# Optimization experiments

Hardware: AMD Instinct MI355X
Metric: run time of the kernel (lower is better)

Reference implementation:

```python
import jax, jax.numpy as jnp
import numpy as np

DIM = 256
HEAD_DIM = 32
GRID = 8
EPS_GN = 1e-6
EPS_LN = 1e-5


def groupnorm1(x, w, b):
    # GroupNorm(1, C): normalize over (C,H,W) per sample, per-channel affine.
    m = jnp.mean(x, axis=(1, 2, 3), keepdims=True)
    v = jnp.var(x, axis=(1, 2, 3), keepdims=True)
    xn = (x - m) * jax.lax.rsqrt(v + EPS_GN)
    return xn * w[None, :, None, None] + b[None, :, None, None]


def conv1x1(x, w, b=None):
    # 1x1 conv as channel matmul; w: [out, in]
    y = jnp.einsum('bchw,oc->bohw', x, w)
    if b is not None:
        y = y + b[None, :, None, None]
    return y


def setup_inputs() -> dict:
    key = jax.random.key(0)
    ks = jax.random.split(key, 8)
    C = DIM
    s = 0.02
    return {
        'x': jax.random.normal(ks[0], (4, C, 64, 64), dtype=jnp.float32),
        'norm_w': jnp.ones((C,), jnp.float32),
        'norm_b': jnp.zeros((C,), jnp.float32),
        'qkv_w': jax.random.normal(ks[1], (3 * C, C), jnp.float32) * s,
        'qkv_b': jnp.zeros((3 * C,), jnp.float32),
        'proj_w': jax.random.normal(ks[2], (C, C), jnp.float32) * s,
        'proj_b': jnp.zeros((C,), jnp.float32),
        'grid_norm_w': jnp.ones((C,), jnp.float32),
        'grid_norm_b': jnp.zeros((C,), jnp.float32),
        'pm_ln_w': jnp.ones((4 * C,), jnp.float32),
        'pm_ln_b': jnp.zeros((4 * C,), jnp.float32),
        'pm_red_w': jax.random.normal(ks[3], (C, 4 * C), jnp.float32) * s,
        'ds_norm_w': jnp.ones((C,), jnp.float32),
        'ds_norm_b': jnp.zeros((C,), jnp.float32),
        'q_w': jax.random.normal(ks[4], (C, C), jnp.float32) * s,
        'q_b': jnp.zeros((C,), jnp.float32),
        'kv_w': jax.random.normal(ks[5], (2 * C, C), jnp.float32) * s,
        'kv_b': jnp.zeros((2 * C,), jnp.float32),
    }


def reference(x, norm_w, norm_b, qkv_w, qkv_b, proj_w, proj_b,
              grid_norm_w, grid_norm_b, pm_ln_w, pm_ln_b, pm_red_w,
              ds_norm_w, ds_norm_b, q_w, q_b, kv_w, kv_b):
    B, C, H, W = x.shape
    hd = HEAD_DIM
    nh = C // hd
    gs = GRID
    gh, gw = H // gs, W // gs
    scale = hd ** -0.5

    # ---- local windowed (grid) attention ----
    qkv = conv1x1(groupnorm1(x, norm_w, norm_b), qkv_w, qkv_b)  # [B,3C,H,W]
    qkv = qkv.reshape(B, 3, nh, hd, gh, gs, gw, gs)
    qkv = qkv.transpose(1, 0, 2, 4, 6, 5, 7, 3).reshape(3, -1, gs * gs, hd)
    q, k, v = qkv[0], qkv[1], qkv[2]
    attn = jax.nn.softmax(jnp.einsum('nqd,nkd->nqk', q * scale, k), axis=-1)
    gx = jnp.einsum('nqk,nkd->nqd', attn, v)
    gx = gx.reshape(B, nh, gh, gw, gs, gs, hd)
    gx = gx.transpose(0, 1, 6, 2, 4, 3, 5).reshape(B, C, H, W)
    grid_x = groupnorm1(x + gx, grid_norm_w, grid_norm_b)

    t = grid_x.transpose(0, 2, 3, 1)  # BHWC
    m = jnp.concatenate([t[:, 0::2, 0::2], t[:, 1::2, 0::2],
                         t[:, 0::2, 1::2], t[:, 1::2, 1::2]], axis=-1)
    m = m.reshape(B, (H // 2) * (W // 2), 4 * C)
    mu = jnp.mean(m, axis=-1, keepdims=True)
    var = jnp.var(m, axis=-1, keepdims=True)
    m = (m - mu) * jax.lax.rsqrt(var + EPS_LN) * pm_ln_w + pm_ln_b
    m = m @ pm_red_w.T  # [B, HW/4, C]
    pm = m.reshape(B, H // 2, W // 2, C).transpose(0, 3, 1, 2)

    # ---- global attention (full q attends to pooled kv) ----
    ds = groupnorm1(pm, ds_norm_w, ds_norm_b)
    qg = conv1x1(grid_x, q_w, q_b).reshape(B, nh, hd, H * W).transpose(0, 1, 3, 2)
    kvg = conv1x1(ds, kv_w, kv_b).reshape(B, 2, nh, hd, (H // 2) * (W // 2))
    kvg = kvg.transpose(1, 0, 2, 4, 3)
    kg, vg = kvg[0], kvg[1]
    attn2 = jax.nn.softmax(jnp.einsum('bnqd,bnkd->bnqk', qg * scale, kg), axis=-1)
    go = jnp.einsum('bnqk,bnkd->bnqd', attn2, vg)
    go = go.transpose(0, 1, 3, 2).reshape(B, C, H, W)
    global_x = go + grid_x

    # drop=0.0 -> identity
    return conv1x1(global_x, proj_w, proj_b)
```

## Files before the change

kernel.cpp:

```cpp
#include <hip/hip_runtime.h>
#include <hip/hip_bf16.h>

#define BATCH 4
#define CDIM 256
#define HWSZ 4096
#define P2 1024
#define SCALE 0.17677669529663687f
#define LOG2E 1.4426950408889634f
#define SCL2 (SCALE * LOG2E)
#define EPS_GN 1e-6f
#define EPS_LN 1e-5f
#define MFIX 8.0f
#define MFIX2 (MFIX * LOG2E)

typedef short v8s __attribute__((ext_vector_type(8)));
typedef float v4f __attribute__((ext_vector_type(4)));

__device__ __forceinline__ unsigned short f2bf(float f) {
    __hip_bfloat16 h = __float2bfloat16(f);
    return *reinterpret_cast<unsigned short*>(&h);
}
__device__ __forceinline__ float bf2f(unsigned short u) {
    return __uint_as_float(((unsigned int)u) << 16);
}
__device__ __forceinline__ float bflo(unsigned int u) {
    return __uint_as_float(u << 16);
}
__device__ __forceinline__ float bfhi(unsigned int u) {
    return __uint_as_float(u & 0xffff0000u);
}
__device__ __forceinline__ unsigned int pack2(float lo, float hi) {
    return (unsigned int)f2bf(lo) | ((unsigned int)f2bf(hi) << 16);
}
__device__ __forceinline__ unsigned int tpack2(float lo, float hi) {
    return (__float_as_uint(lo) >> 16) | (__float_as_uint(hi) & 0xffff0000u);
}
__device__ __forceinline__ float fexp2(float x) {
#if __has_builtin(__builtin_amdgcn_exp2f)
    return __builtin_amdgcn_exp2f(x);
#else
    return exp2f(x);
#endif
}
__device__ __forceinline__ uint2 expack2(v4f s, float& sum) {
    float a = fexp2(s[0] - MFIX2);
    float b = fexp2(s[1] - MFIX2);
    float c = fexp2(s[2] - MFIX2);
    float d = fexp2(s[3] - MFIX2);
    sum += (a + b) + (c + d);
    return make_uint2(tpack2(a, b), tpack2(c, d));
}
__device__ __forceinline__ v8s u4v8(uint2 a, uint2 b) {
    union { unsigned int u[4]; v8s v; } r;
    r.u[0] = a.x; r.u[1] = a.y; r.u[2] = b.x; r.u[3] = b.y;
    return r.v;
}
__device__ __forceinline__ int vperm(int j) {
    return (j & 0x23) | ((j & 0x0C) << 1) | ((j & 0x10) >> 2);
}
__device__ __forceinline__ void async16(void* lds, const void* g) {
    __builtin_amdgcn_global_load_lds(
        (const __attribute__((address_space(1))) unsigned int*)g,
        (__attribute__((address_space(3))) unsigned int*)lds, 16, 0, 0);
}

__global__ void gn_partial4(const float* __restrict__ a, const unsigned short* __restrict__ a2bf,
                            int pb4, int nblk, float* __restrict__ part)
{
    int bb  = blockIdx.x / nblk;
    int blk = blockIdx.x % nblk;
    const float* pa = a + (size_t)bb * pb4 * 4;
    const unsigned short* pa2 = a2bf ? a2bf + (size_t)bb * pb4 * 4 : nullptr;
    int tid = threadIdx.x;
    float s = 0.f, s2 = 0.f;
    for (int i = blk * 256 + tid; i < pb4; i += nblk * 256) {
        float4 v = *(const float4*)(pa + (size_t)i * 4);
        if (pa2) {
            uint2 g = *(const uint2*)(pa2 + (size_t)i * 4);
            v.x += bflo(g.x); v.y += bfhi(g.x);
            v.z += bflo(g.y); v.w += bfhi(g.y);
        }
        s += (v.x + v.y) + (v.z + v.w);
        s2 += fmaf(v.x, v.x, fmaf(v.y, v.y, fmaf(v.z, v.z, v.w * v.w)));
    }
    __shared__ float ls[256], ls2[256];
    ls[tid] = s; ls2[tid] = s2; __syncthreads();
    for (int off = 128; off > 0; off >>= 1) {
        if (tid < off) { ls[tid] += ls[tid + off]; ls2[tid] += ls2[tid + off]; }
        __syncthreads();
    }
    if (tid == 0) {
        part[blockIdx.x * 2]     = ls[0];
        part[blockIdx.x * 2 + 1] = ls2[0];
    }
}

__global__ void cast_weights(const float* __restrict__ w0, const float* __restrict__ w1,
                             const float* __restrict__ w2, const float* __restrict__ w3,
                             const float* __restrict__ w4, unsigned short* __restrict__ dst)
{
    int i = blockIdx.x * 256 + threadIdx.x;
    int idx = i * 4;
    const float* src; int off;
    if      (idx < 196608) { src = w0; off = 0; }
    else if (idx < 458752) { src = w1; off = 196608; }
    else if (idx < 589824) { src = w2; off = 458752; }
    else if (idx < 655360) { src = w3; off = 589824; }
    else                   { src = w4; off = 655360; }
    float4 v = *(const float4*)(src + idx - off);
    *(uint2*)(dst + idx) = make_uint2(pack2(v.x, v.y), pack2(v.z, v.w));
}

__global__ __launch_bounds__(256) void tnc(
    const float* __restrict__ A, const unsigned short* __restrict__ A2b,
    const float* __restrict__ part, int nblk, float inv_n, float eps,
    const float* __restrict__ nw, const float* __restrict__ nb,
    unsigned short* __restrict__ dst, int P)
{
    int b = blockIdx.z, c0 = blockIdx.y * 64, p0 = blockIdx.x * 64;
    __shared__ float ld[64][65];
    __shared__ float sstat[2];
    int t = threadIdx.x;
    if (t < 64) {
        float s = 0.f, s2 = 0.f;
        if (t < nblk) {
            s  = part[(b * nblk + t) * 2];
            s2 = part[(b * nblk + t) * 2 + 1];
        }
        #pragma unroll
        for (int off = 32; off > 0; off >>= 1) {
            s  += __shfl_down(s, off);
            s2 += __shfl_down(s2, off);
        }
        if (t == 0) {
            float mval = s * inv_n;
            float var  = s2 * inv_n - mval * mval;
            sstat[0] = mval;
            sstat[1] = rsqrtf(var + eps);
        }
    }
    __syncthreads();
    float mean = sstat[0], rstd = sstat[1];
    {
        int ch = t >> 2, pq = (t & 3) * 16;
        size_t base = ((size_t)b * 256 + c0 + ch) * P + p0 + pq;
        float4 f0 = *(const float4*)(A + base);
        float4 f1 = *(const float4*)(A + base + 4);
        float4 f2 = *(const float4*)(A + base + 8);
        float4 f3 = *(const float4*)(A + base + 12);
        if (A2b) {
            const unsigned short* ap = A2b + base;
            uint4 q0 = *(const uint4*)(ap);
            uint4 q1 = *(const uint4*)(ap + 8);
            f0.x += bflo(q0.x); f0.y += bfhi(q0.x); f0.z += bflo(q0.y); f0.w += bfhi(q0.y);
            f1.x += bflo(q0.z); f1.y += bfhi(q0.z); f1.z += bflo(q0.w); f1.w += bfhi(q0.w);
            f2.x += bflo(q1.x); f2.y += bfhi(q1.x); f2.z += bflo(q1.y); f2.w += bfhi(q1.y);
            f3.x += bflo(q1.z); f3.y += bfhi(q1.z); f3.z += bflo(q1.w); f3.w += bfhi(q1.w);
        }
        float wv = nw[c0 + ch];
        float sw = rstd * wv;
        float sb = nb[c0 + ch] - mean * rstd * wv;
        ld[ch][pq + 0]  = f0.x * sw + sb; ld[ch][pq + 1]  = f0.y * sw + sb;
        ld[ch][pq + 2]  = f0.z * sw + sb; ld[ch][pq + 3]  = f0.w * sw + sb;
        ld[ch][pq + 4]  = f1.x * sw + sb; ld[ch][pq + 5]  = f1.y * sw + sb;
        ld[ch][pq + 6]  = f1.z * sw + sb; ld[ch][pq + 7]  = f1.w * sw + sb;
        ld[ch][pq + 8]  = f2.x * sw + sb; ld[ch][pq + 9]  = f2.y * sw + sb;
        ld[ch][pq + 10] = f2.z * sw + sb; ld[ch][pq + 11] = f2.w * sw + sb;
        ld[ch][pq + 12] = f3.x * sw + sb; ld[ch][pq + 13] = f3.y * sw + sb;
        ld[ch][pq + 14] = f3.z * sw + sb; ld[ch][pq + 15] = f3.w * sw + sb;
    }
    __syncthreads();
    {
        int p = t >> 2, cb = (t & 3) * 16;
        unsigned int u[8];
        #pragma unroll
        for (int j = 0; j < 8; j++)
            u[j] = pack2(ld[cb + 2 * j][p], ld[cb + 2 * j + 1][p]);
        unsigned short* dp = dst + ((size_t)b * P + p0 + p) * 256 + c0 + cb;
        *(uint4*)(dp)     = make_uint4(u[0], u[1], u[2], u[3]);
        *(uint4*)(dp + 8) = make_uint4(u[4], u[5], u[6], u[7]);
    }
}

template<int MODE>
__global__ __launch_bounds__(256, 3) void gemm_bf16(
    const unsigned short* __restrict__ actT,
    const unsigned short* __restrict__ Wb,
    const float* __restrict__ bias,
    float* __restrict__ out,
    unsigned short* __restrict__ aux1,
    unsigned short* __restrict__ aux2,
    int K, int P, int OC, float oscale)
{
    int b  = blockIdx.z;
    int p0 = blockIdx.x * 128;
    int m0 = blockIdx.y * 128;
    int tid = threadIdx.x;
    int w = tid >> 6, lane = tid & 63;
    int lm = lane & 15, lg = lane >> 4;
    int wm = w >> 1, wp = w & 1;
    int l8 = lane >> 3, cc = lane & 7;

    __shared__ __align__(16) unsigned short Wt[128 * 64];
    __shared__ __align__(16) unsigned short At[128 * 64];

    const unsigned short* actB = actT + (size_t)b * P * K;

    v4f acc[4][4];
    #pragma unroll
    for (int i = 0; i < 4; i++)
        #pragma unroll
        for (int j = 0; j < 4; j++) acc[i][j] = (v4f){0.f, 0.f, 0.f, 0.f};

    for (int ks = 0; ks < K; ks += 64) {
        #pragma unroll
        for (int i = 0; i < 4; i++) {
            int ml = w * 32 + i * 8 + l8;
            int g = cc ^ (ml & 7);
            async16(&Wt[ml * 64], Wb + (size_t)(m0 + ml) * K + ks + g * 8);
        }
        #pragma unroll
        for (int i = 0; i < 4; i++) {
            int pl = w * 32 + i * 8 + l8;
            int g = cc ^ (pl & 7);
            async16(&At[pl * 64], actB + (size_t)(p0 + pl) * K + ks + g * 8);
        }
        __syncthreads();
        #pragma unroll
        for (int kk = 0; kk < 2; kk++) {
            v8s af[4], bfv[4];
            #pragma unroll
            for (int mt = 0; mt < 4; mt++) {
                int m = wm * 64 + mt * 16 + lm;
                int ch = (kk * 4 + lg) ^ (m & 7);
                af[mt] = *(const v8s*)&Wt[m * 64 + ch * 8];
            }
            #pragma unroll
            for (int pt = 0; pt < 4; pt++) {
                int p = wp * 64 + pt * 16 + lm;
                int ch = (kk * 4 + lg) ^ (p & 7);
                bfv[pt] = *(const v8s*)&At[p * 64 + ch * 8];
            }
            #pragma unroll
            for (int mt = 0; mt < 4; mt++)
                #pragma unroll
                for (int pt = 0; pt < 4; pt++)
                    acc[mt][pt] = __builtin_amdgcn_mfma_f32_16x16x32_bf16(
                        af[mt], bfv[pt], acc[mt][pt], 0, 0, 0);
        }
        __syncthreads();
    }

    if constexpr (MODE == 1) {
        if (m0 < 512) {
            #pragma unroll
            for (int mt = 0; mt < 4; mt++) {
                int mch = m0 + wm * 64 + mt * 16 + lg * 4;
                float4 bs = *(const float4*)(bias + mch);
                #pragma unroll
                for (int pt = 0; pt < 4; pt++) {
                    int p = p0 + wp * 64 + pt * 16 + lm;
                    unsigned int u0 = pack2(acc[mt][pt][0] + bs.x, acc[mt][pt][1] + bs.y);
                    unsigned int u1 = pack2(acc[mt][pt][2] + bs.z, acc[mt][pt][3] + bs.w);
                    *(uint2*)(aux1 + ((size_t)(b * 4096 + p) * 512 + mch)) = make_uint2(u0, u1);
                }
            }
        } else {
            #pragma unroll
            for (int mt = 0; mt < 4; mt++) {
                #pragma unroll
                for (int r = 0; r < 4; r++) {
                    int mch = m0 + wm * 64 + mt * 16 + lg * 4 + r;
                    float bsv = bias[mch];
                    unsigned short* orow = aux2 + ((size_t)b * 256 + (mch - 512)) * 4096
                                           + p0 + wp * 64;
                    #pragma unroll
                    for (int pt = 0; pt < 4; pt++)
                        orow[pt * 16 + lm] = f2bf(acc[mt][pt][r] + bsv);
                }
            }
        }
    } else if constexpr (MODE == 2) {
        #pragma unroll
        for (int mt = 0; mt < 4; mt++) {
            int ch = m0 + wm * 64 + mt * 16 + lg * 4;
            int head = ch >> 5, d = ch & 31;
            float4 bs = *(const float4*)(bias + ch);
            #pragma unroll
            for (int pt = 0; pt < 4; pt++) {
                int p = p0 + wp * 64 + pt * 16 + lm;
                unsigned int u0 = pack2((acc[mt][pt][0] + bs.x) * oscale,
                                        (acc[mt][pt][1] + bs.y) * oscale);
                unsigned int u1 = pack2((acc[mt][pt][2] + bs.z) * oscale,
                                        (acc[mt][pt][3] + bs.w) * oscale);
                *(uint2*)(aux1 + ((size_t)(b * 8 + head) * P + p) * 32 + d) = make_uint2(u0, u1);
            }
        }
    } else if constexpr (MODE == 3) {
        #pragma unroll
        for (int mt = 0; mt < 4; mt++) {
            int ch = m0 + wm * 64 + mt * 16 + lg * 4;
            if (ch < 256) {
                int head = ch >> 5, d = ch & 31;
                float4 bs = *(const float4*)(bias + ch);
                #pragma unroll
                for (int pt = 0; pt < 4; pt++) {
                    int p = p0 + wp * 64 + pt * 16 + lm;
                    unsigned int u0 = pack2(acc[mt][pt][0] + bs.x, acc[mt][pt][1] + bs.y);
                    unsigned int u1 = pack2(acc[mt][pt][2] + bs.z, acc[mt][pt][3] + bs.w);
                    *(uint2*)(aux1 + ((size_t)(b * 8 + head) * P + p) * 32 + d) = make_uint2(u0, u1);
                }
            } else {
                int v = ch - 256;
                int head = v >> 5, d0 = v & 31;
                #pragma unroll
                for (int pt = 0; pt < 4; pt++) {
                    int p = p0 + wp * 64 + pt * 16 + lm;
                    int pos = (p & ~63) | vperm(p & 63);
                    #pragma unroll
                    for (int r = 0; r < 4; r++)
                        aux2[((size_t)(b * 8 + head) * 32 + d0 + r) * P + pos] =
                            f2bf(acc[mt][pt][r] + bias[ch + r]);
                }
            }
        }
    } else {
        #pragma unroll
        for (int mt = 0; mt < 4; mt++) {
            #pragma unroll
            for (int r = 0; r < 4; r++) {
                int m = m0 + wm * 64 + mt * 16 + lg * 4 + r;
                float bs = bias ? bias[m] : 0.f;
                float* orow = out + (size_t)b * OC * P + (size_t)m * P + p0 + wp * 64;
                #pragma unroll
                for (int pt = 0; pt < 4; pt++)
                    orow[pt * 16 + lm] = acc[mt][pt][r] + bs;
            }
        }
    }
}

__global__ __launch_bounds__(256, 4) void local_attn_mfma(
    const unsigned short* __restrict__ qkp,
    const unsigned short* __restrict__ vbb,
    unsigned short* __restrict__ gxb)
{
    int win = blockIdx.x;
    int gxc = win & 7, gy = (win >> 3) & 7, h = (win >> 6) & 7, b = win >> 9;
    int w = threadIdx.x >> 6, lane = threadIdx.x & 63;
    int m = lane & 15, g = lane >> 4;

    int rowbase = (gy * 8) * 64 + gxc * 8;
    const unsigned short* qkb = qkp + (size_t)b * 4096 * 512;
    const unsigned short* vbase = vbb + (size_t)b * 256 * 4096;

    int tq = w * 16 + m;
    int pq = rowbase + (tq >> 3) * 64 + (tq & 7);
    v8s qf = *(const v8s*)(qkb + (size_t)pq * 512 + h * 32 + g * 8);

    v8s ka[4];
    #pragma unroll
    for (int kt = 0; kt < 4; kt++) {
        int tk = kt * 16 + m;
        int pk = rowbase + (tk >> 3) * 64 + (tk & 7);
        ka[kt] = *(const v8s*)(qkb + (size_t)pk * 512 + 256 + h * 32 + g * 8);
    }
    v8s vb[2][2];
    #pragma unroll
    for (int c = 0; c < 2; c++)
        #pragma unroll
        for (int dt = 0; dt < 2; dt++) {
            const unsigned short* vp = vbase + (size_t)(h * 32 + dt * 16 + m) * 4096
                              + rowbase + (4 * c + (g >> 1)) * 64 + (g & 1) * 4;
            vb[c][dt] = u4v8(*(const uint2*)vp, *(const uint2*)(vp + 128));
        }

    const v4f zf = {0.f, 0.f, 0.f, 0.f};
    v4f s[4];
    #pragma unroll
    for (int kt = 0; kt < 4; kt++)
        s[kt] = __builtin_amdgcn_mfma_f32_16x16x32_bf16(ka[kt], qf, zf, 0, 0, 0);

    float lsum = 0.f;
    uint2 u0, u1, u2, u3;
    {
        v4f sc;
        #pragma unroll
        for (int r = 0; r < 4; r++) sc[r] = s[0][r] * SCL2;
        u0 = expack2(sc, lsum);
        #pragma unroll
        for (int r = 0; r < 4; r++) sc[r] = s[1][r] * SCL2;
        u1 = expack2(sc, lsum);
        #pragma unroll
        for (int r = 0; r < 4; r++) sc[r] = s[2][r] * SCL2;
        u2 = expack2(sc, lsum);
        #pragma unroll
        for (int r = 0; r < 4; r++) sc[r] = s[3][r] * SCL2;
        u3 = expack2(sc, lsum);
    }
    lsum += __shfl_xor(lsum, 16);
    lsum += __shfl_xor(lsum, 32);
    float inv = 1.f / lsum;

    v8s pa0 = u4v8(u0, u1), pa1 = u4v8(u2, u3);
    v4f o0 = zf, o1 = zf;
    o0 = __builtin_amdgcn_mfma_f32_16x16x32_bf16(pa0, vb[0][0], o0, 0, 0, 0);
    o1 = __builtin_amdgcn_mfma_f32_16x16x32_bf16(pa0, vb[0][1], o1, 0, 0, 0);
    o0 = __builtin_amdgcn_mfma_f32_16x16x32_bf16(pa1, vb[1][0], o0, 0, 0, 0);
    o1 = __builtin_amdgcn_mfma_f32_16x16x32_bf16(pa1, vb[1][1], o1, 0, 0, 0);

    float invq[4];
    #pragma unroll
    for (int r = 0; r < 4; r++) invq[r] = __shfl(inv, g * 4 + r);

    int t0 = w * 16 + g * 4;
    int px0 = rowbase + (t0 >> 3) * 64 + (t0 & 7);
    unsigned short* op0 = gxb + ((size_t)b * 256 + h * 32 + m) * 4096 + px0;
    *(uint2*)op0 = make_uint2(pack2(o0[0] * invq[0], o0[1] * invq[1]),
                              pack2(o0[2] * invq[2], o0[3] * invq[3]));
    unsigned short* op1 = gxb + ((size_t)b * 256 + h * 32 + 16 + m) * 4096 + px0;
    *(uint2*)op1 = make_uint2(pack2(o1[0] * invq[0], o1[1] * invq[1]),
                              pack2(o1[2] * invq[2], o1[3] * invq[3]));
}

__global__ __launch_bounds__(256) void patch_merge_ln2(
    const unsigned short* __restrict__ gxT,
    const float* __restrict__ lnw, const float* __restrict__ lnb,
    unsigned short* __restrict__ mn)
{
    int pix = blockIdx.x;
    int b = pix >> 10, op = pix & 1023;
    int oh = op >> 5, ow = op & 31;
    int t = threadIdx.x;
    const unsigned short* base = gxT + (size_t)b * 4096 * 256;
    float v[4];
    #pragma unroll
    for (int i = 0; i < 4; i++) {
        int h = 2 * oh + (i & 1);
        int w = 2 * ow + (i >> 1);
        v[i] = bf2f(base[(size_t)(h * 64 + w) * 256 + t]);
    }
    float s  = v[0] + v[1] + v[2] + v[3];
    float s2 = v[0]*v[0] + v[1]*v[1] + v[2]*v[2] + v[3]*v[3];
    __shared__ float ls[256], ls2[256];
    ls[t] = s; ls2[t] = s2; __syncthreads();
    for (int off = 128; off > 0; off >>= 1) {
        if (t < off) { ls[t] += ls[t + off]; ls2[t] += ls2[t + off]; }
        __syncthreads();
    }
    float mu  = ls[0] * (1.f / 1024.f);
    float var = ls2[0] * (1.f / 1024.f) - mu * mu;
    float r = rsqrtf(var + EPS_LN);
    unsigned short* orow = mn + (size_t)pix * 1024;
    #pragma unroll
    for (int i = 0; i < 4; i++) {
        int j = i * 256 + t;
        orow[j] = f2bf((v[i] - mu) * r * lnw[j] + lnb[j]);
    }
}

__global__ __launch_bounds__(256, 2) void global_attn_mfma(
    const unsigned short* __restrict__ qT,
    const unsigned short* __restrict__ kT,
    const unsigned short* __restrict__ vT,
    const unsigned short* __restrict__ gxT,
    unsigned short* __restrict__ projT)
{
    int blk = blockIdx.x;
    int qt = blk & 15, h = (blk >> 4) & 7, b = blk >> 7;
    int bh = b * 8 + h;
    int w = threadIdx.x >> 6, lane = threadIdx.x & 63;
    int m = lane & 15, g = lane >> 4;
    int qbase = qt * 256 + w * 64;

    const unsigned short* qp = qT + ((size_t)bh * 4096 + qbase + m) * 32 + g * 8;
    v8s qf0 = *(const v8s*)(qp);
    v8s qf1 = *(const v8s*)(qp + 16 * 32);
    v8s qf2 = *(const v8s*)(qp + 32 * 32);
    v8s qf3 = *(const v8s*)(qp + 48 * 32);

    const v4f zf = {0.f, 0.f, 0.f, 0.f};
    v4f o00 = zf, o01 = zf, o10 = zf, o11 = zf;
    v4f o20 = zf, o21 = zf, o30 = zf, o31 = zf;
    float l0 = 0.f, l1 = 0.f, l2 = 0.f, l3 = 0.f;

    const unsigned short* kbase = kT + ((size_t)bh * 1024 + m) * 32 + g * 8;
    const unsigned short* vbase = vT + ((size_t)bh * 32 + m) * 1024 + g * 8;

    v8s ka0 = *(const v8s*)(kbase);
    v8s ka1 = *(const v8s*)(kbase + 16 * 32);
    v8s ka2 = *(const v8s*)(kbase + 32 * 32);
    v8s ka3 = *(const v8s*)(kbase + 48 * 32);
    v8s vb0 = *(const v8s*)(vbase);
    v8s vb1 = *(const v8s*)(vbase + 16 * 1024);
    v8s vb2 = *(const v8s*)(vbase + 32);
    v8s vb3 = *(const v8s*)(vbase + 32 + 16 * 1024);

    #pragma unroll 2
    for (int t = 0; t < 16; t++) {
        int kn = (t < 15 ? t + 1 : 15) * 64;
        const unsigned short* kp = kbase + (size_t)kn * 32;
        const unsigned short* vp = vbase + kn;
        v8s nk0 = *(const v8s*)(kp);
        v8s nk1 = *(const v8s*)(kp + 16 * 32);
        v8s nk2 = *(const v8s*)(kp + 32 * 32);
        v8s nk3 = *(const v8s*)(kp + 48 * 32);
        v8s nv0 = *(const v8s*)(vp);
        v8s nv1 = *(const v8s*)(vp + 16 * 1024);
        v8s nv2 = *(const v8s*)(vp + 32);
        v8s nv3 = *(const v8s*)(vp + 32 + 16 * 1024);
        __builtin_amdgcn_sched_barrier(0);

        {
            v4f s0 = __builtin_amdgcn_mfma_f32_16x16x32_bf16(ka0, qf0, zf, 0, 0, 0);
            v4f s1 = __builtin_amdgcn_mfma_f32_16x16x32_bf16(ka1, qf0, zf, 0, 0, 0);
            v4f s2 = __builtin_amdgcn_mfma_f32_16x16x32_bf16(ka2, qf0, zf, 0, 0, 0);
            v4f s3 = __builtin_amdgcn_mfma_f32_16x16x32_bf16(ka3, qf0, zf, 0, 0, 0);
            uint2 a0 = expack2(s0, l0), a1 = expack2(s1, l0);
            uint2 a2 = expack2(s2, l0), a3 = expack2(s3, l0);
            v8s pa0 = u4v8(a0, a1), pa1 = u4v8(a2, a3);
            o00 = __builtin_amdgcn_mfma_f32_16x16x32_bf16(pa0, vb0, o00, 0, 0, 0);
            o01 = __builtin_amdgcn_mfma_f32_16x16x32_bf16(pa0, vb1, o01, 0, 0, 0);
            o00 = __builtin_amdgcn_mfma_f32_16x16x32_bf16(pa1, vb2, o00, 0, 0, 0);
            o01 = __builtin_amdgcn_mfma_f32_16x16x32_bf16(pa1, vb3, o01, 0, 0, 0);
        }
        {
            v4f s0 = __builtin_amdgcn_mfma_f32_16x16x32_bf16(ka0, qf1, zf, 0, 0, 0);
            v4f s1 = __builtin_amdgcn_mfma_f32_16x16x32_bf16(ka1, qf1, zf, 0, 0, 0);
            v4f s2 = __builtin_amdgcn_mfma_f32_16x16x32_bf16(ka2, qf1, zf, 0, 0, 0);
            v4f s3 = __builtin_amdgcn_mfma_f32_16x16x32_bf16(ka3, qf1, zf, 0, 0, 0);
            uint2 a0 = expack2(s0, l1), a1 = expack2(s1, l1);
            uint2 a2 = expack2(s2, l1), a3 = expack2(s3, l1);
            v8s pa0 = u4v8(a0, a1), pa1 = u4v8(a2, a3);
            o10 = __builtin_amdgcn_mfma_f32_16x16x32_bf16(pa0, vb0, o10, 0, 0, 0);
            o11 = __builtin_amdgcn_mfma_f32_16x16x32_bf16(pa0, vb1, o11, 0, 0, 0);
            o10 = __builtin_amdgcn_mfma_f32_16x16x32_bf16(pa1, vb2, o10, 0, 0, 0);
            o11 = __builtin_amdgcn_mfma_f32_16x16x32_bf16(pa1, vb3, o11, 0, 0, 0);
        }
        {
            v4f s0 = __builtin_amdgcn_mfma_f32_16x16x32_bf16(ka0, qf2, zf, 0, 0, 0);
            v4f s1 = __builtin_amdgcn_mfma_f32_16x16x32_bf16(ka1, qf2, zf, 0, 0, 0);
            v4f s2 = __builtin_amdgcn_mfma_f32_16x16x32_bf16(ka2, qf2, zf, 0, 0, 0);
            v4f s3 = __builtin_amdgcn_mfma_f32_16x16x32_bf16(ka3, qf2, zf, 0, 0, 0);
            uint2 a0 = expack2(s0, l2), a1 = expack2(s1, l2);
            uint2 a2 = expack2(s2, l2), a3 = expack2(s3, l2);
            v8s pa0 = u4v8(a0, a1), pa1 = u4v8(a2, a3);
            o20 = __builtin_amdgcn_mfma_f32_16x16x32_bf16(pa0, vb0, o20, 0, 0, 0);
            o21 = __builtin_amdgcn_mfma_f32_16x16x32_bf16(pa0, vb1, o21, 0, 0, 0);
            o20 = __builtin_amdgcn_mfma_f32_16x16x32_bf16(pa1, vb2, o20, 0, 0, 0);
            o21 = __builtin_amdgcn_mfma_f32_16x16x32_bf16(pa1, vb3, o21, 0, 0, 0);
        }
        {
            v4f s0 = __builtin_amdgcn_mfma_f32_16x16x32_bf16(ka0, qf3, zf, 0, 0, 0);
            v4f s1 = __builtin_amdgcn_mfma_f32_16x16x32_bf16(ka1, qf3, zf, 0, 0, 0);
            v4f s2 = __builtin_amdgcn_mfma_f32_16x16x32_bf16(ka2, qf3, zf, 0, 0, 0);
            v4f s3 = __builtin_amdgcn_mfma_f32_16x16x32_bf16(ka3, qf3, zf, 0, 0, 0);
            uint2 a0 = expack2(s0, l3), a1 = expack2(s1, l3);
            uint2 a2 = expack2(s2, l3), a3 = expack2(s3, l3);
            v8s pa0 = u4v8(a0, a1), pa1 = u4v8(a2, a3);
            o30 = __builtin_amdgcn_mfma_f32_16x16x32_bf16(pa0, vb0, o30, 0, 0, 0);
            o31 = __builtin_amdgcn_mfma_f32_16x16x32_bf16(pa0, vb1, o31, 0, 0, 0);
            o30 = __builtin_amdgcn_mfma_f32_16x16x32_bf16(pa1, vb2, o30, 0, 0, 0);
            o31 = __builtin_amdgcn_mfma_f32_16x16x32_bf16(pa1, vb3, o31, 0, 0, 0);
        }

        ka0 = nk0; ka1 = nk1; ka2 = nk2; ka3 = nk3;
        vb0 = nv0; vb1 = nv1; vb2 = nv2; vb3 = nv3;
    }

    float lf[4] = {l0, l1, l2, l3};
    v4f oq0[4] = {o00, o10, o20, o30};
    v4f oq1[4] = {o01, o11, o21, o31};
    #pragma unroll
    for (int qi = 0; qi < 4; qi++) {
        float lfq = lf[qi];
        lfq += __shfl_xor(lfq, 16);
        lfq += __shfl_xor(lfq, 32);
        float inv = 1.f / lfq;
        float invq[4];
        #pragma unroll
        for (int r = 0; r < 4; r++) invq[r] = __shfl(inv, g * 4 + r);
        #pragma unroll
        for (int r = 0; r < 4; r++) {
            size_t row = ((size_t)b * 4096 + qbase + qi * 16 + g * 4 + r) * 256 + h * 32;
            projT[row + m]      = f2bf(bf2f(gxT[row + m])      + oq0[qi][r] * invq[r]);
            projT[row + 16 + m] = f2bf(bf2f(gxT[row + 16 + m]) + oq1[qi][r] * invq[r]);
        }
    }
}

extern "C" void kernel_launch(void* const* d_in, const int* in_sizes, int n_in,
                              void* d_out, int out_size, void* d_ws, size_t ws_size,
                              hipStream_t stream)
{
    const float* x           = (const float*)d_in[0];
    const float* norm_w      = (const float*)d_in[1];
    const float* norm_b      = (const float*)d_in[2];
    const float* qkv_w       = (const float*)d_in[3];
    const float* qkv_b       = (const float*)d_in[4];
    const float* proj_w      = (const float*)d_in[5];
    const float* proj_b      = (const float*)d_in[6];
    const float* grid_norm_w = (const float*)d_in[7];
    const float* grid_norm_b = (const float*)d_in[8];
    const float* pm_ln_w     = (const float*)d_in[9];
    const float* pm_ln_b     = (const float*)d_in[10];
    const float* pm_red_w    = (const float*)d_in[11];
    const float* ds_norm_w   = (const float*)d_in[12];
    const float* ds_norm_b   = (const float*)d_in[13];
    const float* q_w         = (const float*)d_in[14];
    const float* q_b         = (const float*)d_in[15];
    const float* kv_w        = (const float*)d_in[16];
    const float* kv_b        = (const float*)d_in[17];
    float* out = (float*)d_out;

    float* wsf = (float*)d_ws;
    unsigned short* qkp   = (unsigned short*)(wsf);
    unsigned short* vbb   = (unsigned short*)(wsf + 4194304);
    unsigned short* mnb   = (unsigned short*)(wsf);
    unsigned short* kTu   = (unsigned short*)(wsf);
    unsigned short* vTu   = (unsigned short*)(wsf + 524288);
    float* pm             = wsf + 2097152;
    unsigned short* pmT   = (unsigned short*)(wsf + 3145728);
    unsigned short* qTu   = (unsigned short*)(wsf + 10485760);
    unsigned short* gxb   = (unsigned short*)(wsf + 12582912);
    unsigned short* projT = (unsigned short*)(wsf + 12582912);
    unsigned short* xT    = (unsigned short*)(wsf + 16777216);
    unsigned short* gxT   = (unsigned short*)(wsf + 16777216);
    float* part   = wsf + 18874368;
    unsigned short* wbf   = (unsigned short*)(wsf + 18875392);
    unsigned short* wbf_qkv  = wbf;
    unsigned short* wbf_pm   = wbf + 196608;
    unsigned short* wbf_kv   = wbf + 458752;
    unsigned short* wbf_q    = wbf + 589824;
    unsigned short* wbf_proj = wbf + 655360;

    cast_weights<<<704, 256, 0, stream>>>(qkv_w, pm_red_w, kv_w, q_w, proj_w, wbf);
    gn_partial4<<<BATCH * 64, 256, 0, stream>>>(x, nullptr, 262144, 64, part);
    tnc<<<dim3(64, 4, BATCH), 256, 0, stream>>>(
        x, nullptr, part, 64, 1.f / 1048576.f, EPS_GN, norm_w, norm_b, xT, 4096);
    gemm_bf16<1><<<dim3(32, 6, BATCH), 256, 0, stream>>>(
        xT, wbf_qkv, qkv_b, nullptr, qkp, vbb, 256, 4096, 768, 1.f);
    local_attn_mfma<<<2048, 256, 0, stream>>>(qkp, vbb, gxb);
    gn_partial4<<<BATCH * 64, 256, 0, stream>>>(x, gxb, 262144, 64, part);
    tnc<<<dim3(64, 4, BATCH), 256, 0, stream>>>(
        x, gxb, part, 64, 1.f / 1048576.f, EPS_GN, grid_norm_w, grid_norm_b, gxT, 4096);
    patch_merge_ln2<<<4096, 256, 0, stream>>>(gxT, pm_ln_w, pm_ln_b, mnb);
    gemm_bf16<0><<<dim3(8, 2, BATCH), 256, 0, stream>>>(
        mnb, wbf_pm, nullptr, pm, nullptr, nullptr, 1024, 1024, 256, 1.f);
    gn_partial4<<<BATCH * 16, 256, 0, stream>>>(pm, nullptr, 65536, 16, part);
    tnc<<<dim3(16, 4, BATCH), 256, 0, stream>>>(
        pm, nullptr, part, 16, 1.f / 262144.f, EPS_GN, ds_norm_w, ds_norm_b, pmT, 1024);
    gemm_bf16<3><<<dim3(8, 4, BATCH), 256, 0, stream>>>(
        pmT, wbf_kv, kv_b, nullptr, kTu, vTu, 256, 1024, 512, 1.f);
    gemm_bf16<2><<<dim3(32, 2, BATCH), 256, 0, stream>>>(
        gxT, wbf_q, q_b, nullptr, qTu, nullptr, 256, 4096, 256, SCL2);
    global_attn_mfma<<<512, 256, 0, stream>>>(qTu, kTu, vTu, gxT, projT);
    gemm_bf16<0><<<dim3(32, 2, BATCH), 256, 0, stream>>>(
        projT, wbf_proj, proj_b, out, nullptr, nullptr, 256, 4096, 256, 1.f);
}
```

Baseline: 167.4 us.

## Stage K/V tiles in double-buffered shared memory via async copies in global attention

The global attention kernel stops having every wave load its own K and V fragments from global memory into registers. The block's four waves now cooperatively copy each 64-key K/V tile into a double-buffered LDS area with async 16-byte copies, and the next tile is prefetched while the current one is computed. The V tile uses an XOR swizzle to avoid LDS bank conflicts, and each wave reads its MFMA operands from LDS. This removes redundant global/L1 traffic across waves. In exchange it adds a block-wide barrier every iteration and uses extra LDS, which can constrain scheduling.

```diff
diff --git a/kernel.cpp b/kernel.cpp
--- a/kernel.cpp
+++ b/kernel.cpp
@@ -473,6 +473,9 @@
     int m = lane & 15, g = lane >> 4;
     int qbase = qt * 256 + w * 64;
 
+    __shared__ __align__(16) unsigned short Kl[2][2048];
+    __shared__ __align__(16) unsigned short Vl[2][2048];
+
     const unsigned short* qp = qT + ((size_t)bh * 4096 + qbase + m) * 32 + g * 8;
     v8s qf0 = *(const v8s*)(qp);
     v8s qf1 = *(const v8s*)(qp + 16 * 32);
@@ -484,32 +487,40 @@
     v4f o20 = zf, o21 = zf, o30 = zf, o31 = zf;
     float l0 = 0.f, l1 = 0.f, l2 = 0.f, l3 = 0.f;
 
-    const unsigned short* kbase = kT + ((size_t)bh * 1024 + m) * 32 + g * 8;
-    const unsigned short* vbase = vT + ((size_t)bh * 32 + m) * 1024 + g * 8;
-
-    v8s ka0 = *(const v8s*)(kbase);
-    v8s ka1 = *(const v8s*)(kbase + 16 * 32);
-    v8s ka2 = *(const v8s*)(kbase + 32 * 32);
-    v8s ka3 = *(const v8s*)(kbase + 48 * 32);
-    v8s vb0 = *(const v8s*)(vbase);
-    v8s vb1 = *(const v8s*)(vbase + 16 * 1024);
-    v8s vb2 = *(const v8s*)(vbase + 32);
-    v8s vb3 = *(const v8s*)(vbase + 32 + 16 * 1024);
+    const unsigned short* kB = kT + (size_t)bh * 1024 * 32;
+    const unsigned short* vB = vT + (size_t)bh * 32 * 1024;
+
+    int ck   = w * 64 + lane;
+    int krow = ck >> 2, kslot = ck & 3;
+    int vrow = ck >> 3, vslot = ck & 7;
+    int vgs  = vslot ^ (vrow & 7);
+    size_t ksrc = (size_t)krow * 32 + kslot * 8;
+    size_t vsrc = (size_t)vrow * 1024 + vgs * 8;
+
+    async16(&Kl[0][(size_t)w * 512], kB + ksrc);
+    async16(&Vl[0][(size_t)w * 512], vB + vsrc);
+    __syncthreads();
+
+    int sv = (m & 7);
 
     #pragma unroll 2
     for (int t = 0; t < 16; t++) {
-        int kn = (t < 15 ? t + 1 : 15) * 64;
-        const unsigned short* kp = kbase + (size_t)kn * 32;
-        const unsigned short* vp = vbase + kn;
-        v8s nk0 = *(const v8s*)(kp);
-        v8s nk1 = *(const v8s*)(kp + 16 * 32);
-        v8s nk2 = *(const v8s*)(kp + 32 * 32);
-        v8s nk3 = *(const v8s*)(kp + 48 * 32);
-        v8s nv0 = *(const v8s*)(vp);
-        v8s nv1 = *(const v8s*)(vp + 16 * 1024);
-        v8s nv2 = *(const v8s*)(vp + 32);
-        v8s nv3 = *(const v8s*)(vp + 32 + 16 * 1024);
-        __builtin_amdgcn_sched_barrier(0);
+        if (t < 15) {
+            int k0n = (t + 1) * 64;
+            async16(&Kl[(t + 1) & 1][(size_t)w * 512], kB + (size_t)k0n * 32 + ksrc);
+            async16(&Vl[(t + 1) & 1][(size_t)w * 512], vB + k0n + vsrc);
+        }
+        const unsigned short* Kb = Kl[t & 1];
+        const unsigned short* Vb = Vl[t & 1];
+
+        v8s ka0 = *(const v8s*)&Kb[(0 * 16 + m) * 32 + g * 8];
+        v8s ka1 = *(const v8s*)&Kb[(1 * 16 + m) * 32 + g * 8];
+        v8s ka2 = *(const v8s*)&Kb[(2 * 16 + m) * 32 + g * 8];
+        v8s ka3 = *(const v8s*)&Kb[(3 * 16 + m) * 32 + g * 8];
+        v8s vb0 = *(const v8s*)&Vb[m * 64 + ((g) ^ sv) * 8];
+        v8s vb1 = *(const v8s*)&Vb[(m + 16) * 64 + ((g) ^ sv) * 8];
+        v8s vb2 = *(const v8s*)&Vb[m * 64 + ((4 + g) ^ sv) * 8];
+        v8s vb3 = *(const v8s*)&Vb[(m + 16) * 64 + ((4 + g) ^ sv) * 8];
 
         {
             v4f s0 = __builtin_amdgcn_mfma_f32_16x16x32_bf16(ka0, qf0, zf, 0, 0, 0);
@@ -564,8 +575,7 @@
             o31 = __builtin_amdgcn_mfma_f32_16x16x32_bf16(pa1, vb3, o31, 0, 0, 0);
         }
 
-        ka0 = nk0; ka1 = nk1; ka2 = nk2; ka3 = nk3;
-        vb0 = nv0; vb1 = nv1; vb2 = nv2; vb3 = nv3;
+        __syncthreads();
     }
 
     float lf[4] = {l0, l1, l2, l3};
```

New measurement: 172.0 us. 1.03x slower.
